# Kernel tuning notes

Measured on AMD Instinct MI355X. Metric: run time of the kernel, lower is better.

Reference implementation:

```python
import jax, jax.numpy as jnp
import numpy as np

B, N, C, H, W = 8, 64, 256, 100, 100
PROJ_C, HID, EMB = 256, 128, 64
GN_EPS = 1e-5
NORM_EPS = 1e-6


def setup_inputs() -> dict:
    key = jax.random.key(0)
    ks = jax.random.split(key, 8)
    features = jax.random.normal(ks[0], (B, C, H, W), dtype=jnp.float32)
    boxes_xyxy = jax.random.uniform(ks[1], (B, N, 4), dtype=jnp.float32)  # normalized boxes in [0,1]
    conv_w = jax.random.normal(ks[2], (PROJ_C, C), dtype=jnp.float32) * (1.0 / np.sqrt(C))  # 1x1 conv, no bias
    gn_w = jnp.ones((PROJ_C,), dtype=jnp.float32)
    gn_b = jnp.zeros((PROJ_C,), dtype=jnp.float32)
    w1 = jax.random.normal(ks[3], (PROJ_C, HID), dtype=jnp.float32) * (1.0 / np.sqrt(PROJ_C))
    b1 = jnp.zeros((HID,), dtype=jnp.float32)
    w2 = jax.random.normal(ks[4], (HID, EMB), dtype=jnp.float32) * (1.0 / np.sqrt(HID))
    b2 = jnp.zeros((EMB,), dtype=jnp.float32)
    return {"features": features, "boxes_xyxy": boxes_xyxy, "conv_w": conv_w,
            "gn_w": gn_w, "gn_b": gn_b, "w1": w1, "b1": b1, "w2": w2, "b2": b2}


def _silu(x):
    return x * jax.nn.sigmoid(x)


def _forward(features, boxes_xyxy, conv_w, gn_w, gn_b, w1, b1, w2, b2):
    # feature_proj: 1x1 conv (no bias) -> GroupNorm(groups=1) -> SiLU
    y = jnp.einsum('bchw,oc->bohw', features, conv_w)
    mu = y.mean(axis=(1, 2, 3), keepdims=True)
    var = y.var(axis=(1, 2, 3), keepdims=True)
    y = (y - mu) * jax.lax.rsqrt(var + GN_EPS)
    y = y * gn_w[None, :, None, None] + gn_b[None, :, None, None]
    src = _silu(y)  # [B,PROJ_C,H,W]

    # project normalized boxes to feature coords (normalized_boxes=True)
    x1 = jnp.minimum(boxes_xyxy[..., 0], boxes_xyxy[..., 2]) * W
    x2 = jnp.maximum(boxes_xyxy[..., 0], boxes_xyxy[..., 2]) * W
    y1 = jnp.minimum(boxes_xyxy[..., 1], boxes_xyxy[..., 3]) * H
    y2 = jnp.maximum(boxes_xyxy[..., 1], boxes_xyxy[..., 3]) * H
    x1 = jnp.clip(jnp.floor(jnp.clip(x1, 0.0, W)), 0.0, W)
    x2 = jnp.clip(jnp.ceil(jnp.clip(x2, 0.0, W)), 0.0, W)
    y1 = jnp.clip(jnp.floor(jnp.clip(y1, 0.0, H)), 0.0, H)
    y2 = jnp.clip(jnp.ceil(jnp.clip(y2, 0.0, H)), 0.0, H)

    # separable region masks: region is rows y1:y2, cols x1:x2
    hs = jnp.arange(H, dtype=jnp.float32)
    ws = jnp.arange(W, dtype=jnp.float32)
    my = ((hs >= y1[..., None]) & (hs < y2[..., None])).astype(src.dtype)  # [B,N,H]
    mx = ((ws >= x1[..., None]) & (ws < x2[..., None])).astype(src.dtype)  # [B,N,W]

    region_sum = jnp.einsum('bnh,bnw,bchw->bnc', my, mx, src)
    count = my.sum(-1) * mx.sum(-1)  # [B,N]
    pooled = jnp.where(count[..., None] > 0, region_sum / jnp.maximum(count[..., None], 1.0), 0.0)

    # embedding MLP + L2 normalize (torch F.normalize semantics)
    raw = _silu(pooled @ w1 + b1) @ w2 + b2
    norm = jnp.linalg.norm(raw, axis=-1, keepdims=True)
    emb = raw / jnp.maximum(norm, NORM_EPS)
    return emb, raw, pooled


def reference(features, boxes_xyxy, conv_w, gn_w, gn_b, w1, b1, w2, b2):
    return _forward(features, boxes_xyxy, conv_w, gn_w, gn_b, w1, b1, w2, b2)
```

## Files before the change

### kernel.cpp

```cpp
#include <hip/hip_runtime.h>
#include <hip/hip_bf16.h>
#include <math.h>

#define HWq 10000
#define Cq 256
#define Oq 256

typedef __attribute__((ext_vector_type(8))) short short8v;
typedef __attribute__((ext_vector_type(4))) float f32x4;

__device__ __forceinline__ short f2bf(float f) {
    __hip_bfloat16 h = __float2bfloat16(f);
    return *reinterpret_cast<short*>(&h);
}
__device__ __forceinline__ float bf2f(unsigned short u) {
    return __uint_as_float((unsigned)u << 16);
}

__device__ __forceinline__ int swz(int row, int g) {
    return g ^ (row & 3) ^ ((row >> 2) & 1);
}

__global__ __launch_bounds__(256) void conv_mfma(const float* __restrict__ feat,
                                                 const float* __restrict__ convw,
                                                 unsigned short* __restrict__ y,
                                                 float* __restrict__ stats) {
    __shared__ __align__(16) short Albuf[64 * 32];
    __shared__ __align__(16) short Blbuf[128 * 32];
    __shared__ float redbuf[8];

    const int b  = blockIdx.z;
    const int o0 = blockIdx.y * 64;
    const int p0 = blockIdx.x * 128;
    const int t  = threadIdx.x;
    const int w  = t >> 6;
    const int l  = t & 63;
    const int wo = (w >> 1) * 32;
    const int wp = (w & 1) * 64;

    const float* fb = feat + (size_t)b * Cq * HWq;

    f32x4 acc[2][4];
    #pragma unroll
    for (int i = 0; i < 2; ++i)
        #pragma unroll
        for (int j = 0; j < 4; ++j)
            acc[i][j] = (f32x4){0.f, 0.f, 0.f, 0.f};

    const int oA  = t >> 2;
    const int kuA = t & 3;
    const float* aptr = convw + (size_t)(o0 + oA) * Cq + kuA * 8;

    int pgB[2];
    #pragma unroll
    for (int pass = 0; pass < 2; ++pass) {
        int pg = p0 + pass * 64 + l;
        pgB[pass] = (pg > HWq - 1) ? (HWq - 1) : pg;
    }

    const int fr_g = l >> 4;
    const int fr_r = l & 15;

    float4 ra0, ra1;
    float  rb[2][8];

    auto LOADG = [&](int k0) {
        ra0 = *(const float4*)(aptr + k0);
        ra1 = *(const float4*)(aptr + k0 + 4);
        #pragma unroll
        for (int pass = 0; pass < 2; ++pass) {
            const float* fk = fb + (size_t)(k0 + w * 8) * HWq + pgB[pass];
            #pragma unroll
            for (int jj = 0; jj < 8; ++jj)
                rb[pass][jj] = fk[(size_t)jj * HWq];
        }
    };

    LOADG(0);

    for (int k0 = 0; k0 < Cq; k0 += 32) {
        if (k0) __syncthreads();

        {
            short8v s;
            s[0]=f2bf(ra0.x); s[1]=f2bf(ra0.y); s[2]=f2bf(ra0.z); s[3]=f2bf(ra0.w);
            s[4]=f2bf(ra1.x); s[5]=f2bf(ra1.y); s[6]=f2bf(ra1.z); s[7]=f2bf(ra1.w);
            *(short8v*)((char*)Albuf + oA * 64 + swz(oA, kuA) * 16) = s;
            #pragma unroll
            for (int pass = 0; pass < 2; ++pass) {
                short8v sb;
                #pragma unroll
                for (int jj = 0; jj < 8; ++jj) sb[jj] = f2bf(rb[pass][jj]);
                int p = pass * 64 + l;
                *(short8v*)((char*)Blbuf + p * 64 + swz(p, w) * 16) = sb;
            }
        }
        __syncthreads();

        if (k0 < Cq - 32) LOADG(k0 + 32);

        short8v af[2], bfv[4];
        #pragma unroll
        for (int i = 0; i < 2; ++i) {
            int row = wo + i * 16 + fr_r;
            af[i] = *(const short8v*)((const char*)Albuf + row * 64 + swz(row, fr_g) * 16);
        }
        #pragma unroll
        for (int j = 0; j < 4; ++j) {
            int row = wp + j * 16 + fr_r;
            bfv[j] = *(const short8v*)((const char*)Blbuf + row * 64 + swz(row, fr_g) * 16);
        }
        #pragma unroll
        for (int i = 0; i < 2; ++i)
            #pragma unroll
            for (int j = 0; j < 4; ++j)
                acc[i][j] = __builtin_amdgcn_mfma_f32_16x16x32_bf16(af[i], bfv[j], acc[i][j], 0, 0, 0);
    }

    float lsum = 0.f, lsq = 0.f;
    #pragma unroll
    for (int i = 0; i < 2; ++i) {
        const int obase = o0 + wo + i * 16 + (l >> 4) * 4;
        #pragma unroll
        for (int j = 0; j < 4; ++j) {
            const int p = p0 + wp + j * 16 + (l & 15);
            if (p < HWq) {
                #pragma unroll
                for (int r = 0; r < 4; ++r) {
                    float v = acc[i][j][r];
                    y[((size_t)(b * Oq + obase + r)) * HWq + p] = (unsigned short)f2bf(v);
                    lsum += v;
                    lsq  += v * v;
                }
            }
        }
    }
    #pragma unroll
    for (int m = 1; m < 64; m <<= 1) {
        lsum += __shfl_xor(lsum, m);
        lsq  += __shfl_xor(lsq, m);
    }
    if (l == 0) { redbuf[w] = lsum; redbuf[4 + w] = lsq; }
    __syncthreads();
    if (t == 0) {
        atomicAdd(&stats[b],     redbuf[0] + redbuf[1] + redbuf[2] + redbuf[3]);
        atomicAdd(&stats[8 + b], redbuf[4] + redbuf[5] + redbuf[6] + redbuf[7]);
    }
}

__global__ __launch_bounds__(512) void integral_pool(const unsigned short* __restrict__ y,
                                                     const float* __restrict__ boxes,
                                                     const float* __restrict__ stats,
                                                     const float* __restrict__ gnw,
                                                     const float* __restrict__ gnb,
                                                     float* __restrict__ pooled) {
    __shared__ float Sl[10000];

    const int plane = blockIdx.x;
    const int b = plane >> 8;
    const int c = plane & 255;
    const int wave = threadIdx.x >> 6;
    const int lane = threadIdx.x & 63;

    const float invM = 1.f / 2560000.f;
    const float mu   = stats[b] * invM;
    const float msq  = stats[8 + b] * invM;
    const float rs   = rsqrtf(msq - mu * mu + 1e-5f);
    const float scale = gnw[c] * rs;
    const float shift = gnb[c] - mu * scale;

    const unsigned short* yp = y + (size_t)plane * HWq;

    for (int i = 0; i < 13; i += 2) {
        const int r0 = wave + 8 * i;
        const int r1 = r0 + 8;
        const bool has0 = r0 < 100;
        const bool has1 = r1 < 100;
        float a0 = 0.f, b0 = 0.f, a1 = 0.f, b1 = 0.f;
        if (lane < 50) {
            if (has0) {
                ushort2 u0 = *(const ushort2*)(yp + r0 * 100 + 2 * lane);
                float v0 = bf2f(u0.x) * scale + shift;
                float v1 = bf2f(u0.y) * scale + shift;
                a0 = v0 / (1.f + __expf(-v0));
                b0 = v1 / (1.f + __expf(-v1));
            }
            if (has1) {
                ushort2 u1 = *(const ushort2*)(yp + r1 * 100 + 2 * lane);
                float w0 = bf2f(u1.x) * scale + shift;
                float w1 = bf2f(u1.y) * scale + shift;
                a1 = w0 / (1.f + __expf(-w0));
                b1 = w1 / (1.f + __expf(-w1));
            }
        }
        float p0 = a0 + b0;
        float p1 = a1 + b1;
        #pragma unroll
        for (int m = 1; m < 64; m <<= 1) {
            float t0 = __shfl_up(p0, m);
            float t1 = __shfl_up(p1, m);
            if (lane >= m) { p0 += t0; p1 += t1; }
        }
        if (lane < 50) {
            if (has0) {
                float2 o0 = {p0 - b0, p0};
                *(float2*)(&Sl[r0 * 100 + 2 * lane]) = o0;
            }
            if (has1) {
                float2 o1 = {p1 - b1, p1};
                *(float2*)(&Sl[r1 * 100 + 2 * lane]) = o1;
            }
        }
    }
    __syncthreads();

    {
        const int grp = lane >> 3;
        const int j   = lane & 7;
        const int n   = wave * 8 + grp;
        const float4 bx = *(const float4*)(boxes + ((size_t)b * 64 + n) * 4);

        float x1f = fminf(bx.x, bx.z) * 100.f;
        float x2f = fmaxf(bx.x, bx.z) * 100.f;
        float y1f = fminf(bx.y, bx.w) * 100.f;
        float y2f = fmaxf(bx.y, bx.w) * 100.f;
        x1f = fminf(fmaxf(floorf(fminf(fmaxf(x1f, 0.f), 100.f)), 0.f), 100.f);
        x2f = fminf(fmaxf(ceilf (fminf(fmaxf(x2f, 0.f), 100.f)), 0.f), 100.f);
        y1f = fminf(fmaxf(floorf(fminf(fmaxf(y1f, 0.f), 100.f)), 0.f), 100.f);
        y2f = fminf(fmaxf(ceilf (fminf(fmaxf(y2f, 0.f), 100.f)), 0.f), 100.f);
        const int ix1 = (int)x1f, ix2 = (int)x2f;
        const int iy1 = (int)y1f, iy2 = (int)y2f;
        const int cnt = (ix2 - ix1) * (iy2 - iy1);

        float v = 0.f;
        if (cnt > 0) {
            const int colR = ix2 - 1;
            const int colL = ix1 - 1;
            for (int h = iy1 + j; h < iy2; h += 8) {
                float s = Sl[h * 100 + colR];
                if (colL >= 0) s -= Sl[h * 100 + colL];
                v += s;
            }
        }
        v += __shfl_xor(v, 1);
        v += __shfl_xor(v, 2);
        v += __shfl_xor(v, 4);
        if (j == 0)
            pooled[((size_t)b * 64 + n) * Cq + c] = (cnt > 0) ? v / (float)cnt : 0.f;
    }
}

__global__ __launch_bounds__(128) void mlp_kernel(const float* __restrict__ pooled,
                                                  const float* __restrict__ w1,
                                                  const float* __restrict__ b1,
                                                  const float* __restrict__ w2,
                                                  const float* __restrict__ b2,
                                                  float* __restrict__ emb,
                                                  float* __restrict__ raw) {
    __shared__ float ps[256];
    __shared__ float hs[128];
    const int bn = blockIdx.x;
    const int t  = threadIdx.x;

    ps[t]       = pooled[(size_t)bn * 256 + t];
    ps[t + 128] = pooled[(size_t)bn * 256 + t + 128];
    __syncthreads();

    float a0 = 0.f, a1 = 0.f, a2 = 0.f, a3 = 0.f;
    #pragma unroll 4
    for (int c = 0; c < 256; c += 4) {
        a0 += ps[c]     * w1[c * 128 + t];
        a1 += ps[c + 1] * w1[(c + 1) * 128 + t];
        a2 += ps[c + 2] * w1[(c + 2) * 128 + t];
        a3 += ps[c + 3] * w1[(c + 3) * 128 + t];
    }
    float a = b1[t] + ((a0 + a1) + (a2 + a3));
    hs[t] = a / (1.f + __expf(-a));
    __syncthreads();

    if (t < 64) {
        float r0 = 0.f, r1 = 0.f, r2 = 0.f, r3 = 0.f;
        #pragma unroll 4
        for (int h = 0; h < 128; h += 4) {
            r0 += hs[h]     * w2[h * 64 + t];
            r1 += hs[h + 1] * w2[(h + 1) * 64 + t];
            r2 += hs[h + 2] * w2[(h + 2) * 64 + t];
            r3 += hs[h + 3] * w2[(h + 3) * 64 + t];
        }
        float r = b2[t] + ((r0 + r1) + (r2 + r3));
        raw[(size_t)bn * 64 + t] = r;
        float s = r * r;
        #pragma unroll
        for (int m = 1; m < 64; m <<= 1) s += __shfl_xor(s, m);
        float nrm = fmaxf(sqrtf(s), 1e-6f);
        emb[(size_t)bn * 64 + t] = r / nrm;
    }
}

extern "C" void kernel_launch(void* const* d_in, const int* in_sizes, int n_in,
                              void* d_out, int out_size, void* d_ws, size_t ws_size,
                              hipStream_t stream) {
    const float* feat  = (const float*)d_in[0];
    const float* boxes = (const float*)d_in[1];
    const float* convw = (const float*)d_in[2];
    const float* gnw   = (const float*)d_in[3];
    const float* gnb   = (const float*)d_in[4];
    const float* w1    = (const float*)d_in[5];
    const float* b1    = (const float*)d_in[6];
    const float* w2    = (const float*)d_in[7];
    const float* b2    = (const float*)d_in[8];

    float* out    = (float*)d_out;
    float* emb    = out;
    float* raw    = out + 32768;
    float* pooled = out + 65536;

    unsigned short* y = (unsigned short*)d_ws;
    float* stats = (float*)((char*)d_ws + (size_t)8 * 256 * 10000 * 2);

    hipMemsetAsync(stats, 0, 16 * sizeof(float), stream);

    dim3 g1((HWq + 127) / 128, 4, 8);
    conv_mfma<<<g1, 256, 0, stream>>>(feat, convw, y, stats);

    integral_pool<<<2048, 512, 0, stream>>>(y, boxes, stats, gnw, gnb, pooled);

    mlp_kernel<<<512, 128, 0, stream>>>(pooled, w1, b1, w2, b2, emb, raw);
}
```

Measured before the change: 243.0 us.

## Enlarge conv output tile to 128 channels with 512-thread blocks

Each conv GEMM block now covers 128 output channels instead of 64 and runs 8 waves, so the feature tile loaded from global memory is shared by twice as many outputs. This halves the number of times the fp32 feature map is re-read from global memory across the output-channel grid dimension. The tradeoff is fewer blocks, more shared memory per block and larger workgroups, which may lower occupancy. The wave-to-tile mapping (wo/wp) is in lines not shown, so whether it covers all 8 waves correctly cannot be confirmed.

```diff
diff --git a/kernel.cpp b/kernel.cpp
--- a/kernel.cpp
+++ b/kernel.cpp
@@ -21,16 +21,16 @@
     return g ^ (row & 3) ^ ((row >> 2) & 1);
 }
 
-__global__ __launch_bounds__(256) void conv_mfma(const float* __restrict__ feat,
+__global__ __launch_bounds__(512) void conv_mfma(const float* __restrict__ feat,
                                                  const float* __restrict__ convw,
                                                  unsigned short* __restrict__ y,
                                                  float* __restrict__ stats) {
-    __shared__ __align__(16) short Albuf[64 * 32];
+    __shared__ __align__(16) short Albuf[128 * 32];
     __shared__ __align__(16) short Blbuf[128 * 32];
-    __shared__ float redbuf[8];
+    __shared__ float redbuf[16];
 
     const int b  = blockIdx.z;
-    const int o0 = blockIdx.y * 64;
+    const int o0 = blockIdx.y * 128;
     const int p0 = blockIdx.x * 128;
     const int t  = threadIdx.x;
     const int w  = t >> 6;
@@ -51,29 +51,24 @@
     const int kuA = t & 3;
     const float* aptr = convw + (size_t)(o0 + oA) * Cq + kuA * 8;
 
-    int pgB[2];
-    #pragma unroll
-    for (int pass = 0; pass < 2; ++pass) {
-        int pg = p0 + pass * 64 + l;
-        pgB[pass] = (pg > HWq - 1) ? (HWq - 1) : pg;
-    }
+    const int pB  = t & 127;
+    const int kgB = t >> 7;
+    int pgB = p0 + pB;
+    if (pgB > HWq - 1) pgB = HWq - 1;
 
     const int fr_g = l >> 4;
     const int fr_r = l & 15;
 
     float4 ra0, ra1;
-    float  rb[2][8];
+    float  rb[8];
 
     auto LOADG = [&](int k0) {
         ra0 = *(const float4*)(aptr + k0);
         ra1 = *(const float4*)(aptr + k0 + 4);
-        #pragma unroll
-        for (int pass = 0; pass < 2; ++pass) {
-            const float* fk = fb + (size_t)(k0 + w * 8) * HWq + pgB[pass];
-            #pragma unroll
-            for (int jj = 0; jj < 8; ++jj)
-                rb[pass][jj] = fk[(size_t)jj * HWq];
-        }
+        const float* fk = fb + (size_t)(k0 + kgB * 8) * HWq + pgB;
+        #pragma unroll
+        for (int jj = 0; jj < 8; ++jj)
+            rb[jj] = fk[(size_t)jj * HWq];
     };
 
     LOADG(0);
@@ -86,14 +81,10 @@
             s[0]=f2bf(ra0.x); s[1]=f2bf(ra0.y); s[2]=f2bf(ra0.z); s[3]=f2bf(ra0.w);
             s[4]=f2bf(ra1.x); s[5]=f2bf(ra1.y); s[6]=f2bf(ra1.z); s[7]=f2bf(ra1.w);
             *(short8v*)((char*)Albuf + oA * 64 + swz(oA, kuA) * 16) = s;
+            short8v sb;
             #pragma unroll
-            for (int pass = 0; pass < 2; ++pass) {
-                short8v sb;
-                #pragma unroll
-                for (int jj = 0; jj < 8; ++jj) sb[jj] = f2bf(rb[pass][jj]);
-                int p = pass * 64 + l;
-                *(short8v*)((char*)Blbuf + p * 64 + swz(p, w) * 16) = sb;
-            }
+            for (int jj = 0; jj < 8; ++jj) sb[jj] = f2bf(rb[jj]);
+            *(short8v*)((char*)Blbuf + pB * 64 + swz(pB, kgB) * 16) = sb;
         }
         __syncthreads();
 
@@ -140,11 +131,14 @@
         lsum += __shfl_xor(lsum, m);
         lsq  += __shfl_xor(lsq, m);
     }
-    if (l == 0) { redbuf[w] = lsum; redbuf[4 + w] = lsq; }
+    if (l == 0) { redbuf[w] = lsum; redbuf[8 + w] = lsq; }
     __syncthreads();
     if (t == 0) {
-        atomicAdd(&stats[b],     redbuf[0] + redbuf[1] + redbuf[2] + redbuf[3]);
-        atomicAdd(&stats[8 + b], redbuf[4] + redbuf[5] + redbuf[6] + redbuf[7]);
+        float s0 = 0.f, s1 = 0.f;
+        #pragma unroll
+        for (int i = 0; i < 8; ++i) { s0 += redbuf[i]; s1 += redbuf[8 + i]; }
+        atomicAdd(&stats[b], s0);
+        atomicAdd(&stats[8 + b], s1);
     }
 }
 
@@ -320,8 +314,8 @@
 
     hipMemsetAsync(stats, 0, 16 * sizeof(float), stream);
 
-    dim3 g1((HWq + 127) / 128, 4, 8);
-    conv_mfma<<<g1, 256, 0, stream>>>(feat, convw, y, stats);
+    dim3 g1((HWq + 127) / 128, 2, 8);
+    conv_mfma<<<g1, 512, 0, stream>>>(feat, convw, y, stats);
 
     integral_pool<<<2048, 512, 0, stream>>>(y, boxes, stats, gnw, gnb, pooled);
 
```

New measurement: 212.7 us. 12.5% less time.
